# Optimization experiments

Hardware: AMD Instinct MI355X
Metric: run time of the kernel (lower is better)

Reference implementation:

```python
import jax, jax.numpy as jnp
import numpy as np
import math
from jax import lax

EPS = 1e-5  # BatchNorm1d default eps
K = 7       # causal conv kernel size
H = 5       # number of heads in block 2


def _cconv(x, w, b):
    # CausalConv1d: left-pad by (K-1)*dilation = 6, then valid conv. x: [B,C,L], w: [O,I,K]
    y = lax.conv_general_dilated(x, w, window_strides=(1,), padding=[(K - 1, 0)],
                                 dimension_numbers=('NCH', 'OIH', 'NCH'))
    return y + b[None, :, None]


def _bn(x, g, b):
    # BatchNorm1d in training mode: batch stats over (N, L) per channel, biased variance
    m = x.mean((0, 2), keepdims=True)
    v = ((x - m) ** 2).mean((0, 2), keepdims=True)
    return g[None, :, None] * (x - m) * lax.rsqrt(v + EPS) + b[None, :, None]


def _attn(x1, x2, x3, scale):
    # sigmoid(((X1 @ X2^T) / sqrt(L)) @ X3); x*: [B,C,L]
    s = jnp.einsum('bcl,bdl->bcd', x1, x2) * scale
    return jax.nn.sigmoid(jnp.einsum('bcd,bdl->bcl', s, x3))


def _attn_heads(x1, x2, x3, scale):
    # 5 heads chunked along L (contiguous chunks) -> vectorized over head axis
    B, C, L = x1.shape
    r = lambda x: x.reshape(B, C, H, L // H)
    x1r, x2r, x3r = r(x1), r(x2), r(x3)
    s = jnp.einsum('bchk,bdhk->bhcd', x1r, x2r) * scale  # scale uses full L, as in source
    a = jax.nn.sigmoid(jnp.einsum('bhcd,bdhk->bchk', s, x3r))
    return a.reshape(B, C, L)


def setup_inputs() -> dict:
    key = jax.random.key(0)
    ks = jax.random.split(key, 20)
    B, C, L = 64, 30, 200
    CL = C * L
    cs = (C * K) ** -0.5   # conv weight scale
    ls = CL ** -0.5        # linear weight scale
    d = {}
    d['X'] = jax.random.normal(ks[0], (B, C, L), jnp.float32)
    for i, nm in enumerate(['b1c1', 'b1c2', 'b1c3', 'b2c1', 'b2c2', 'b2c3']):
        d[nm + '_w'] = jax.random.normal(ks[1 + i], (C, C, K), jnp.float32) * cs
        d[nm + '_b'] = jax.random.normal(ks[7 + i], (C,), jnp.float32) * cs
    for nm in ['bn11', 'bn12', 'bn21', 'bn22']:
        d[nm + '_g'] = jnp.ones((C,), jnp.float32)
        d[nm + '_b'] = jnp.zeros((C,), jnp.float32)
    d['lin1_w'] = jax.random.normal(ks[13], (CL, CL), jnp.float32) * ls
    d['lin1_b'] = jax.random.normal(ks[14], (CL,), jnp.float32) * ls
    d['lin2_w'] = jax.random.normal(ks[15], (CL, CL), jnp.float32) * ls
    d['lin2_b'] = jax.random.normal(ks[16], (CL,), jnp.float32) * ls
    d['cw'] = jax.random.normal(ks[17], (CL, 2 * CL), jnp.float32) * (2 * CL) ** -0.5
    d['cb'] = jax.random.normal(ks[18], (CL,), jnp.float32) * (2 * CL) ** -0.5
    return d


def reference(X, b1c1_w, b1c1_b, b1c2_w, b1c2_b, b1c3_w, b1c3_b,
              bn11_g, bn11_b, lin1_w, lin1_b, lin2_w, lin2_b, bn12_g, bn12_b,
              b2c1_w, b2c1_b, b2c2_w, b2c2_b, b2c3_w, b2c3_b,
              bn21_g, bn21_b, bn22_g, bn22_b, cw, cb):
    B, C, L = X.shape
    scale = 1.0 / math.sqrt(L)
    # block 1: single-head sigmoid attention
    a1 = _attn(_cconv(X, b1c1_w, b1c1_b), _cconv(X, b1c2_w, b1c2_b),
               _cconv(X, b1c3_w, b1c3_b), scale)
    a1 = _bn(a1 + X, bn11_g, bn11_b)
    a1f = a1.reshape(B, -1)
    o1 = (a1f @ lin1_w.T + lin1_b) @ lin2_w.T + lin2_b  # dropout is eval-mode identity
    out1 = _bn(a1 + o1.reshape(B, C, L), bn12_g, bn12_b)
    # block 2: 5-head sigmoid attention
    a2 = _attn_heads(_cconv(X, b2c1_w, b2c1_b), _cconv(X, b2c2_w, b2c2_b),
                     _cconv(X, b2c3_w, b2c3_b), scale)
    a2 = _bn(a2 + X, bn21_g, bn21_b)
    a2f = a2.reshape(B, -1)
    # NOTE: source reuses b1_linearchain for block 2 (b2_linearchain is unused)
    o2 = (a2f @ lin1_w.T + lin1_b) @ lin2_w.T + lin2_b
    out2 = _bn(a2 + o2.reshape(B, C, L), bn22_g, bn22_b)
    # converge
    out = jnp.concatenate([out1, out2], axis=1).reshape(B, -1)  # [B, 2*C*L]
    out = out @ cw.T + cb                                       # [B, C*L]
    return out.reshape(B, 30, -1)
```

## Files before the change

### kernel.cpp

```cpp
#include <hip/hip_runtime.h>
#include <hip/hip_bf16.h>
#include <math.h>

typedef __attribute__((ext_vector_type(4))) float f32x4;
typedef __attribute__((ext_vector_type(8))) __bf16 bf16x8;
typedef __attribute__((ext_vector_type(8))) unsigned short u16x8;

__device__ __forceinline__ unsigned short f2bfu(float f) {
    unsigned u = __builtin_bit_cast(unsigned, f);
    u += 0x7fffu + ((u >> 16) & 1u);
    return (unsigned short)(u >> 16);
}

__device__ __forceinline__ bf16x8 to_bf8(f32x4 x, f32x4 y) {
    bf16x8 o;
#pragma unroll
    for (int j = 0; j < 4; ++j) { o[j] = (__bf16)x[j]; o[j + 4] = (__bf16)y[j]; }
    return o;
}

__device__ __forceinline__ void gload_lds16(const void* g, void* l) {
    __builtin_amdgcn_global_load_lds(
        (__attribute__((address_space(1))) const void*)g,
        (__attribute__((address_space(3))) void*)l, 16, 0, 0);
}

template <int VMPS>
__device__ __forceinline__ void wait_newer(int newer) {
    if (newer >= 2) {
        if constexpr (VMPS == 4) asm volatile("s_waitcnt vmcnt(8)" ::: "memory");
        else                     asm volatile("s_waitcnt vmcnt(6)" ::: "memory");
    } else if (newer == 1) {
        if constexpr (VMPS == 4) asm volatile("s_waitcnt vmcnt(4)" ::: "memory");
        else                     asm volatile("s_waitcnt vmcnt(3)" ::: "memory");
    } else {
        asm volatile("s_waitcnt vmcnt(0)" ::: "memory");
    }
}

struct ConvArgs {
    const float* w[6];
    const float* b[6];
};

__global__ __launch_bounds__(256) void conv_all(const float* __restrict__ X,
                                                ConvArgs args,
                                                float* __restrict__ out) {
    __shared__ float Xsp[30][208];
    __shared__ float Wg[30][212];
    const int b = blockIdx.x, j = blockIdx.y;
    const int tid = threadIdx.x;
    const float* xb = X + (size_t)b * 6000;
    for (int i = tid; i < 30 * 208; i += 256) {
        const int ci = i / 208, p = i - ci * 208;
        float v = 0.f;
        if (p >= 6 && p < 206) v = xb[ci * 200 + (p - 6)];
        Xsp[ci][p] = v;
    }
    const float* wsrc = args.w[j];
    for (int i = tid; i < 6300; i += 256) Wg[i / 210][i % 210] = wsrc[i];
    __syncthreads();
    if (tid < 240) {
        const int c = tid >> 3;
        const int strip = tid & 7;
        const int l0 = strip * 25;
        float acc[25];
        const float bias = args.b[j][c];
#pragma unroll
        for (int o = 0; o < 25; ++o) acc[o] = bias;
        for (int ci = 0; ci < 30; ++ci) {
            float wv[7];
#pragma unroll
            for (int kk = 0; kk < 7; ++kk) wv[kk] = Wg[c][ci * 7 + kk];
            float xw[31];
#pragma unroll
            for (int i = 0; i < 31; ++i) xw[i] = Xsp[ci][l0 + i];
#pragma unroll
            for (int o = 0; o < 25; ++o) {
                float a = acc[o];
#pragma unroll
                for (int kk = 0; kk < 7; ++kk) a += xw[o + kk] * wv[kk];
                acc[o] = a;
            }
        }
        float* op = out + ((size_t)j * 64 + b) * 6000 + c * 200 + l0;
#pragma unroll
        for (int o = 0; o < 25; ++o) op[o] = acc[o];
    }
}

__global__ __launch_bounds__(256) void attn_k(const float* __restrict__ conv,
                                              const float* __restrict__ X,
                                              float* __restrict__ A_lin) {
    __shared__ float x1s[30][204], x2s[30][204], x3s[30][204];
    __shared__ float S[5][30][30];
    const int b = blockIdx.x, blk = blockIdx.y;
    const int tid = threadIdx.x;
    const f32x4* c1 = (const f32x4*)(conv + (((size_t)blk * 3 + 0) * 64 + b) * 6000);
    const f32x4* c2 = (const f32x4*)(conv + (((size_t)blk * 3 + 1) * 64 + b) * 6000);
    const f32x4* c3 = (const f32x4*)(conv + (((size_t)blk * 3 + 2) * 64 + b) * 6000);
    for (int i = tid; i < 1500; i += 256) {
        const int c = i / 50, q = i - c * 50;
        *(f32x4*)&x1s[c][q * 4] = c1[i];
        *(f32x4*)&x2s[c][q * 4] = c2[i];
        *(f32x4*)&x3s[c][q * 4] = c3[i];
    }
    __syncthreads();
    const float scale = 7.0710678118654752e-2f;
    if (blk == 0) {
        for (int idx = tid; idx < 900; idx += 256) {
            const int c = idx / 30, d = idx - c * 30;
            f32x4 a4 = {};
            for (int q = 0; q < 50; ++q) {
                const f32x4 x = *(const f32x4*)&x1s[c][q * 4];
                const f32x4 y = *(const f32x4*)&x2s[d][q * 4];
                a4 += x * y;
            }
            S[0][c][d] = (a4[0] + a4[1] + a4[2] + a4[3]) * scale;
        }
    } else {
        for (int idx = tid; idx < 4500; idx += 256) {
            const int h = idx / 900, rem = idx - h * 900;
            const int c = rem / 30, d = rem - c * 30;
            f32x4 a4 = {};
            for (int q = 0; q < 10; ++q) {
                const f32x4 x = *(const f32x4*)&x1s[c][h * 40 + q * 4];
                const f32x4 y = *(const f32x4*)&x2s[d][h * 40 + q * 4];
                a4 += x * y;
            }
            S[h][c][d] = (a4[0] + a4[1] + a4[2] + a4[3]) * scale;
        }
    }
    __syncthreads();
    const float* Xb = X + (size_t)b * 6000;
    float* Ab = A_lin + ((size_t)blk * 64 + b) * 6000;
    for (int u = tid; u < 1500; u += 256) {
        const int c = u / 50, q = u - c * 50;
        const int hh = (blk == 0) ? 0 : (q / 10);
        f32x4 a4 = {};
        for (int d = 0; d < 30; ++d) {
            const float sv = S[hh][c][d];
            const f32x4 v = *(const f32x4*)&x3s[d][q * 4];
            a4 += sv * v;
        }
        const f32x4 xv = *(const f32x4*)(Xb + c * 200 + q * 4);
        f32x4 o;
#pragma unroll
        for (int jj = 0; jj < 4; ++jj)
            o[jj] = 1.f / (1.f + __expf(-a4[jj])) + xv[jj];
        *(f32x4*)(Ab + c * 200 + q * 4) = o;
    }
}

__global__ __launch_bounds__(256) void bn_stage1(float* __restrict__ A,
                                                 unsigned short* __restrict__ Ab,
                                                 const float* __restrict__ g11,
                                                 const float* __restrict__ b11,
                                                 const float* __restrict__ g21,
                                                 const float* __restrict__ b21) {
    const int c = blockIdx.x, h = blockIdx.y;
    const int tid = threadIdx.x;
    const size_t base = (size_t)h * 64 * 6000 + c * 200;
    float s = 0.f, ss = 0.f;
    for (int i = tid; i < 12800; i += 256) {
        const int b = i / 200, l = i - b * 200;
        const float v = A[base + (size_t)b * 6000 + l];
        s += v; ss += v * v;
    }
    __shared__ float rs[4], rss[4];
    __shared__ float sc_sh, sh_sh;
    for (int off = 32; off > 0; off >>= 1) { s += __shfl_down(s, off); ss += __shfl_down(ss, off); }
    const int wave = tid >> 6, lane = tid & 63;
    if (lane == 0) { rs[wave] = s; rss[wave] = ss; }
    __syncthreads();
    if (tid == 0) {
        const float S = rs[0] + rs[1] + rs[2] + rs[3];
        const float SS = rss[0] + rss[1] + rss[2] + rss[3];
        const float mean = S * (1.f / 12800.f);
        const float var = SS * (1.f / 12800.f) - mean * mean;
        const float* gp = h ? g21 : g11;
        const float* bp = h ? b21 : b11;
        const float scale = gp[c] * rsqrtf(var + 1e-5f);
        sc_sh = scale;
        sh_sh = bp[c] - mean * scale;
    }
    __syncthreads();
    const float scale = sc_sh, shift = sh_sh;
    for (int i = tid; i < 12800; i += 256) {
        const int b = i / 200, l = i - b * 200;
        const size_t idx = base + (size_t)b * 6000 + l;
        const float o = A[idx] * scale + shift;
        A[idx] = o;
        Ab[(size_t)(h * 64 + b) * 6016 + c * 200 + l] = f2bfu(o);
    }
    if (c == 0) {
        for (int i = tid; i < 64 * 16; i += 256)
            Ab[(size_t)(h * 64 + (i >> 4)) * 6016 + 6000 + (i & 15)] = 0;
    }
}

__global__ __launch_bounds__(256) void bn_stage2(const float* __restrict__ A,
                                                 const float* __restrict__ O,
                                                 unsigned short* __restrict__ Cat,
                                                 const float* __restrict__ g12,
                                                 const float* __restrict__ b12,
                                                 const float* __restrict__ g22,
                                                 const float* __restrict__ b22) {
    const int c = blockIdx.x, h = blockIdx.y;
    const int tid = threadIdx.x;
    const size_t base = (size_t)h * 64 * 6000 + c * 200;
    float s = 0.f, ss = 0.f;
    for (int i = tid; i < 12800; i += 256) {
        const int b = i / 200, l = i - b * 200;
        const size_t idx = base + (size_t)b * 6000 + l;
        const float v = A[idx] + O[idx];
        s += v; ss += v * v;
    }
    __shared__ float rs[4], rss[4];
    __shared__ float sc_sh, sh_sh;
    for (int off = 32; off > 0; off >>= 1) { s += __shfl_down(s, off); ss += __shfl_down(ss, off); }
    const int wave = tid >> 6, lane = tid & 63;
    if (lane == 0) { rs[wave] = s; rss[wave] = ss; }
    __syncthreads();
    if (tid == 0) {
        const float S = rs[0] + rs[1] + rs[2] + rs[3];
        const float SS = rss[0] + rss[1] + rss[2] + rss[3];
        const float mean = S * (1.f / 12800.f);
        const float var = SS * (1.f / 12800.f) - mean * mean;
        const float* gp = h ? g22 : g12;
        const float* bp = h ? b22 : b12;
        const float scale = gp[c] * rsqrtf(var + 1e-5f);
        sc_sh = scale;
        sh_sh = bp[c] - mean * scale;
    }
    __syncthreads();
    const float scale = sc_sh, shift = sh_sh;
    for (int i = tid; i < 12800; i += 256) {
        const int b = i / 200, l = i - b * 200;
        const size_t idx = base + (size_t)b * 6000 + l;
        const float o = (A[idx] + O[idx]) * scale + shift;
        Cat[(size_t)b * 12000 + (size_t)h * 6000 + c * 200 + l] = f2bfu(o);
    }
}

template <int MT>
__global__ __launch_bounds__(256) void gemm_pipe(const unsigned short* __restrict__ A,
                                                 const float* __restrict__ W,
                                                 unsigned short* __restrict__ P,
                                                 int N, int K, int KA,
                                                 int iters_total, int iters_per) {
    constexpr int M = MT * 16;
    constexpr int WB = 64 * 32 * 4;
    constexpr int AB = M * 32 * 2;
    constexpr int ACH = AB / 1024;
    constexpr int BUFSZ = WB + AB;
    constexpr int VMPS = 2 + ACH / 4;
    __shared__ __align__(16) char lds[3][BUFSZ];

    const int tid = threadIdx.x;
    const int wave = tid >> 6;
    const int lane = tid & 63;
    const int r = lane & 15;
    const int g = lane >> 4;
    const int n0 = blockIdx.x * 64;
    const int s = blockIdx.y;
    const int it0 = s * iters_per;
    int it1 = it0 + iters_per;
    if (it1 > iters_total) it1 = iters_total;
    const int nst = it1 - it0;

    f32x4 acc[MT] = {};

    auto stage = [&](char* base, int it) {
        const int k0 = it * 32;
#pragma unroll
        for (int u = 0; u < 2; ++u) {
            const int c = wave + 4 * u;
            const int slot = c * 64 + lane;
            const int row = slot >> 3, jj = slot & 7;
            const int j = jj ^ (row & 7);
            int kc = k0 + j * 4;
            if (kc + 4 > K) kc = K - 4;
            int rn = n0 + row;
            if (rn > N - 1) rn = N - 1;
            gload_lds16(W + (size_t)rn * K + kc, base + c * 1024);
        }
        char* abase = base + WB;
#pragma unroll
        for (int u = 0; u < ACH / 4; ++u) {
            const int c = wave + 4 * u;
            const int slot = c * 64 + lane;
            const int m = slot >> 2, jj = slot & 3;
            const int j = jj ^ ((m >> 1) & 3);
            const int kc = k0 + j * 8;
            gload_lds16(A + (size_t)m * KA + kc, abase + c * 1024);
        }
    };

    auto compute = [&](const char* base) {
        const float* Wb = (const float*)base;
        const unsigned short* Ab = (const unsigned short*)(base + WB);
        const int wr = wave * 16 + r;
        const f32x4* Wrow = (const f32x4*)(Wb + wr * 32);
        const f32x4 x = Wrow[(2 * g) ^ (r & 7)];
        const f32x4 y = Wrow[(2 * g + 1) ^ (r & 7)];
        const bf16x8 bfrag = to_bf8(x, y);
#pragma unroll
        for (int mt = 0; mt < MT; ++mt) {
            const int m = mt * 16 + r;
            const bf16x8 afrag = __builtin_bit_cast(
                bf16x8, ((const u16x8*)(Ab + (size_t)m * 32))[g ^ ((m >> 1) & 3)]);
            acc[mt] = __builtin_amdgcn_mfma_f32_16x16x32_bf16(afrag, bfrag, acc[mt], 0, 0, 0);
        }
    };

    if (nst > 0) {
        const int p = nst < 3 ? nst : 3;
        for (int i = 0; i < p; ++i) stage(&lds[i][0], it0 + i);
        wait_newer<VMPS>(p - 1);
        __builtin_amdgcn_s_barrier();
        __builtin_amdgcn_sched_barrier(0);

        int bi = 0;
        for (int it = it0; it < it1; ++it) {
            compute(&lds[bi][0]);
            __builtin_amdgcn_sched_barrier(0);
            __builtin_amdgcn_s_barrier();
            if (it + 3 < it1) stage(&lds[bi][0], it + 3);
            if (it + 1 < it1) {
                const int newer = (it + 3 <= it1 - 1) ? 2 : (it1 - 1) - (it + 1);
                wait_newer<VMPS>(newer);
                __builtin_amdgcn_s_barrier();
                __builtin_amdgcn_sched_barrier(0);
            }
            bi = bi == 2 ? 0 : bi + 1;
        }
    }

    unsigned short* Pp = P + (size_t)s * M * N;
    const int col = n0 + wave * 16 + r;
#pragma unroll
    for (int mt = 0; mt < MT; ++mt) {
#pragma unroll
        for (int rr = 0; rr < 4; ++rr) {
            const int row = mt * 16 + g * 4 + rr;
            if (col < N) Pp[(size_t)row * N + col] = f2bfu(acc[mt][rr]);
        }
    }
}

template <bool OUT_BF16>
__global__ __launch_bounds__(256) void reduce_bias(const unsigned short* __restrict__ P,
                                                   const float* __restrict__ bias,
                                                   int KS, int MN, int N, int KOUT,
                                                   float* __restrict__ of,
                                                   unsigned short* __restrict__ ob) {
    const int gid0 = blockIdx.x * 256 + threadIdx.x;
    const int gstr = gridDim.x * 256;
    for (int idx = gid0; idx < MN; idx += gstr) {
        float v = bias[idx % N];
        for (int s = 0; s < KS; ++s) {
            const unsigned u = P[(size_t)s * MN + idx];
            v += __builtin_bit_cast(float, u << 16);
        }
        if constexpr (OUT_BF16) ob[(size_t)(idx / N) * KOUT + (idx % N)] = f2bfu(v);
        else of[idx] = v;
    }
    if constexpr (OUT_BF16) {
        if (KOUT > N) {
            const int M = MN / N, PADW = KOUT - N;
            for (int i = gid0; i < M * PADW; i += gstr)
                ob[(size_t)(i / PADW) * KOUT + N + (i % PADW)] = 0;
        }
    }
}

extern "C" void kernel_launch(void* const* d_in, const int* in_sizes, int n_in,
                              void* d_out, int out_size, void* d_ws, size_t ws_size,
                              hipStream_t stream) {
    (void)in_sizes; (void)n_in; (void)out_size;
    const float* X = (const float*)d_in[0];
    ConvArgs ca;
    for (int j = 0; j < 6; ++j) {
        ca.w[j] = (const float*)d_in[1 + 2 * j];
        ca.b[j] = (const float*)d_in[2 + 2 * j];
    }
    const float* bn11_g = (const float*)d_in[13];
    const float* bn11_b = (const float*)d_in[14];
    const float* bn12_g = (const float*)d_in[15];
    const float* bn12_b = (const float*)d_in[16];
    const float* bn21_g = (const float*)d_in[17];
    const float* bn21_b = (const float*)d_in[18];
    const float* bn22_g = (const float*)d_in[19];
    const float* bn22_b = (const float*)d_in[20];
    const float* lin1_w = (const float*)d_in[21];
    const float* lin1_b = (const float*)d_in[22];
    const float* lin2_w = (const float*)d_in[23];
    const float* lin2_b = (const float*)d_in[24];
    const float* cw = (const float*)d_in[25];
    const float* cb = (const float*)d_in[26];
    float* out = (float*)d_out;

    char* w = (char*)d_ws;
    float* A_lin = (float*)w;
    unsigned short* A_bf = (unsigned short*)(w + 3072000);
    char* U = w + 4612096;
    float* convout = (float*)U;
    unsigned short* T_bf = (unsigned short*)U;
    float* O = (float*)(U + 1540096);
    unsigned short* Cat = (unsigned short*)(U + 4612096);
    unsigned short* P = (unsigned short*)(w + 13828096);

    const size_t avail = ws_size > 13828096 ? ws_size - 13828096 : 0;
    int KS12 = (int)(avail / 1536000);
    if (KS12 > 8) KS12 = 8;
    if (KS12 < 1) KS12 = 1;
    int KS3 = (int)(avail / 768000);
    if (KS3 > 10) KS3 = 10;
    if (KS3 < 1) KS3 = 1;

    conv_all<<<dim3(64, 6), 256, 0, stream>>>(X, ca, convout);
    attn_k<<<dim3(64, 2), 256, 0, stream>>>(convout, X, A_lin);
    bn_stage1<<<dim3(30, 2), 256, 0, stream>>>(A_lin, A_bf, bn11_g, bn11_b, bn21_g, bn21_b);

    {
        const int it_tot = 188;
        const int it_per = (it_tot + KS12 - 1) / KS12;
        gemm_pipe<8><<<dim3(94, KS12), 256, 0, stream>>>(A_bf, lin1_w, P, 6000, 6000, 6016, it_tot, it_per);
        reduce_bias<true><<<dim3(768), 256, 0, stream>>>(P, lin1_b, KS12, 768000, 6000, 6016, nullptr, T_bf);
        gemm_pipe<8><<<dim3(94, KS12), 256, 0, stream>>>(T_bf, lin2_w, P, 6000, 6000, 6016, it_tot, it_per);
        reduce_bias<false><<<dim3(768), 256, 0, stream>>>(P, lin2_b, KS12, 768000, 6000, 6000, O, nullptr);
    }

    bn_stage2<<<dim3(30, 2), 256, 0, stream>>>(A_lin, O, Cat, bn12_g, bn12_b, bn22_g, bn22_b);

    {
        const int it_tot = 375;
        const int it_per = (it_tot + KS3 - 1) / KS3;
        gemm_pipe<4><<<dim3(94, KS3), 256, 0, stream>>>(Cat, cw, P, 6000, 12000, 12000, it_tot, it_per);
        reduce_bias<false><<<dim3(768), 256, 0, stream>>>(P, cb, KS3, 384000, 6000, 6000, out, nullptr);
    }
}
```

Measured before the change: 282.5 us.

## Widen GEMM N-tile to 128, double-buffer, split BN into stats/apply

The GEMM now has each block cover 128 output columns instead of 64. Each wave holds two B fragments, so every A fragment read from LDS feeds two MFMAs. The pipeline goes from three LDS buffers to two, and the split-K caps rise to 12 and 16 to keep enough blocks with half as many N tiles. BatchNorm is split into a partial-statistics kernel and an apply kernel over a 30x2x8 grid instead of 60 blocks, so the bandwidth-bound normalization uses more CUs. In exchange the pipeline prefetches less deeply, the reduce kernels read more partial sums, and the GEMM uses more accumulator registers.

```diff
diff --git a/kernel.cpp b/kernel.cpp
--- a/kernel.cpp
+++ b/kernel.cpp
@@ -25,17 +25,11 @@
         (__attribute__((address_space(3))) void*)l, 16, 0, 0);
 }
 
-template <int VMPS>
-__device__ __forceinline__ void wait_newer(int newer) {
-    if (newer >= 2) {
-        if constexpr (VMPS == 4) asm volatile("s_waitcnt vmcnt(8)" ::: "memory");
-        else                     asm volatile("s_waitcnt vmcnt(6)" ::: "memory");
-    } else if (newer == 1) {
-        if constexpr (VMPS == 4) asm volatile("s_waitcnt vmcnt(4)" ::: "memory");
-        else                     asm volatile("s_waitcnt vmcnt(3)" ::: "memory");
-    } else {
-        asm volatile("s_waitcnt vmcnt(0)" ::: "memory");
-    }
+template <int N>
+__device__ __forceinline__ void waitcnt_vm() {
+    if constexpr (N == 6)      asm volatile("s_waitcnt vmcnt(6)" ::: "memory");
+    else if constexpr (N == 5) asm volatile("s_waitcnt vmcnt(5)" ::: "memory");
+    else                       asm volatile("s_waitcnt vmcnt(0)" ::: "memory");
 }
 
 struct ConvArgs {
@@ -152,92 +146,89 @@
     }
 }
 
-__global__ __launch_bounds__(256) void bn_stage1(float* __restrict__ A,
+template <bool ADD>
+__global__ __launch_bounds__(256) void bn_stats(const float* __restrict__ A,
+                                                const float* __restrict__ O,
+                                                float* __restrict__ part) {
+    const int c = blockIdx.x, h = blockIdx.y, bs = blockIdx.z;
+    const int tid = threadIdx.x;
+    float s = 0.f, ss = 0.f;
+    for (int i = tid; i < 1600; i += 256) {
+        const int b = bs * 8 + i / 200, l = i % 200;
+        const size_t idx = ((size_t)h * 64 + b) * 6000 + c * 200 + l;
+        float v = A[idx];
+        if constexpr (ADD) v += O[idx];
+        s += v; ss += v * v;
+    }
+    for (int off = 32; off > 0; off >>= 1) { s += __shfl_down(s, off); ss += __shfl_down(ss, off); }
+    __shared__ float rs[4], rss[4];
+    const int wave = tid >> 6, lane = tid & 63;
+    if (lane == 0) { rs[wave] = s; rss[wave] = ss; }
+    __syncthreads();
+    if (tid == 0) {
+        float* p = part + (((size_t)h * 30 + c) * 8 + bs) * 2;
+        p[0] = rs[0] + rs[1] + rs[2] + rs[3];
+        p[1] = rss[0] + rss[1] + rss[2] + rss[3];
+    }
+}
+
+__global__ __launch_bounds__(256) void bn_apply1(float* __restrict__ A,
                                                  unsigned short* __restrict__ Ab,
+                                                 const float* __restrict__ part,
                                                  const float* __restrict__ g11,
                                                  const float* __restrict__ b11,
                                                  const float* __restrict__ g21,
                                                  const float* __restrict__ b21) {
-    const int c = blockIdx.x, h = blockIdx.y;
-    const int tid = threadIdx.x;
-    const size_t base = (size_t)h * 64 * 6000 + c * 200;
-    float s = 0.f, ss = 0.f;
-    for (int i = tid; i < 12800; i += 256) {
-        const int b = i / 200, l = i - b * 200;
-        const float v = A[base + (size_t)b * 6000 + l];
-        s += v; ss += v * v;
-    }
-    __shared__ float rs[4], rss[4];
-    __shared__ float sc_sh, sh_sh;
-    for (int off = 32; off > 0; off >>= 1) { s += __shfl_down(s, off); ss += __shfl_down(ss, off); }
-    const int wave = tid >> 6, lane = tid & 63;
-    if (lane == 0) { rs[wave] = s; rss[wave] = ss; }
-    __syncthreads();
-    if (tid == 0) {
-        const float S = rs[0] + rs[1] + rs[2] + rs[3];
-        const float SS = rss[0] + rss[1] + rss[2] + rss[3];
-        const float mean = S * (1.f / 12800.f);
-        const float var = SS * (1.f / 12800.f) - mean * mean;
-        const float* gp = h ? g21 : g11;
-        const float* bp = h ? b21 : b11;
-        const float scale = gp[c] * rsqrtf(var + 1e-5f);
-        sc_sh = scale;
-        sh_sh = bp[c] - mean * scale;
-    }
-    __syncthreads();
-    const float scale = sc_sh, shift = sh_sh;
-    for (int i = tid; i < 12800; i += 256) {
-        const int b = i / 200, l = i - b * 200;
-        const size_t idx = base + (size_t)b * 6000 + l;
+    const int c = blockIdx.x, h = blockIdx.y, bs = blockIdx.z;
+    const int tid = threadIdx.x;
+    const float* p = part + (((size_t)h * 30 + c) * 8) * 2;
+    float S = 0.f, SS = 0.f;
+#pragma unroll
+    for (int k = 0; k < 8; ++k) { S += p[k * 2]; SS += p[k * 2 + 1]; }
+    const float mean = S * (1.f / 12800.f);
+    const float var = SS * (1.f / 12800.f) - mean * mean;
+    const float* gp = h ? g21 : g11;
+    const float* bp = h ? b21 : b11;
+    const float scale = gp[c] * rsqrtf(var + 1e-5f);
+    const float shift = bp[c] - mean * scale;
+    for (int i = tid; i < 1600; i += 256) {
+        const int b = bs * 8 + i / 200, l = i % 200;
+        const size_t idx = ((size_t)h * 64 + b) * 6000 + c * 200 + l;
         const float o = A[idx] * scale + shift;
         A[idx] = o;
-        Ab[(size_t)(h * 64 + b) * 6016 + c * 200 + l] = f2bfu(o);
+        Ab[((size_t)h * 64 + b) * 6016 + c * 200 + l] = f2bfu(o);
     }
     if (c == 0) {
-        for (int i = tid; i < 64 * 16; i += 256)
-            Ab[(size_t)(h * 64 + (i >> 4)) * 6016 + 6000 + (i & 15)] = 0;
-    }
-}
-
-__global__ __launch_bounds__(256) void bn_stage2(const float* __restrict__ A,
+        for (int i = tid; i < 8 * 16; i += 256) {
+            const int b = bs * 8 + (i >> 4);
+            Ab[((size_t)h * 64 + b) * 6016 + 6000 + (i & 15)] = 0;
+        }
+    }
+}
+
+__global__ __launch_bounds__(256) void bn_apply2(const float* __restrict__ A,
                                                  const float* __restrict__ O,
                                                  unsigned short* __restrict__ Cat,
+                                                 const float* __restrict__ part,
                                                  const float* __restrict__ g12,
                                                  const float* __restrict__ b12,
                                                  const float* __restrict__ g22,
                                                  const float* __restrict__ b22) {
-    const int c = blockIdx.x, h = blockIdx.y;
-    const int tid = threadIdx.x;
-    const size_t base = (size_t)h * 64 * 6000 + c * 200;
-    float s = 0.f, ss = 0.f;
-    for (int i = tid; i < 12800; i += 256) {
-        const int b = i / 200, l = i - b * 200;
-        const size_t idx = base + (size_t)b * 6000 + l;
-        const float v = A[idx] + O[idx];
-        s += v; ss += v * v;
-    }
-    __shared__ float rs[4], rss[4];
-    __shared__ float sc_sh, sh_sh;
-    for (int off = 32; off > 0; off >>= 1) { s += __shfl_down(s, off); ss += __shfl_down(ss, off); }
-    const int wave = tid >> 6, lane = tid & 63;
-    if (lane == 0) { rs[wave] = s; rss[wave] = ss; }
-    __syncthreads();
-    if (tid == 0) {
-        const float S = rs[0] + rs[1] + rs[2] + rs[3];
-        const float SS = rss[0] + rss[1] + rss[2] + rss[3];
-        const float mean = S * (1.f / 12800.f);
-        const float var = SS * (1.f / 12800.f) - mean * mean;
-        const float* gp = h ? g22 : g12;
-        const float* bp = h ? b22 : b12;
-        const float scale = gp[c] * rsqrtf(var + 1e-5f);
-        sc_sh = scale;
-        sh_sh = bp[c] - mean * scale;
-    }
-    __syncthreads();
-    const float scale = sc_sh, shift = sh_sh;
-    for (int i = tid; i < 12800; i += 256) {
-        const int b = i / 200, l = i - b * 200;
-        const size_t idx = base + (size_t)b * 6000 + l;
+    const int c = blockIdx.x, h = blockIdx.y, bs = blockIdx.z;
+    const int tid = threadIdx.x;
+    const float* p = part + (((size_t)h * 30 + c) * 8) * 2;
+    float S = 0.f, SS = 0.f;
+#pragma unroll
+    for (int k = 0; k < 8; ++k) { S += p[k * 2]; SS += p[k * 2 + 1]; }
+    const float mean = S * (1.f / 12800.f);
+    const float var = SS * (1.f / 12800.f) - mean * mean;
+    const float* gp = h ? g22 : g12;
+    const float* bp = h ? b22 : b12;
+    const float scale = gp[c] * rsqrtf(var + 1e-5f);
+    const float shift = bp[c] - mean * scale;
+    for (int i = tid; i < 1600; i += 256) {
+        const int b = bs * 8 + i / 200, l = i % 200;
+        const size_t idx = ((size_t)h * 64 + b) * 6000 + c * 200 + l;
         const float o = (A[idx] + O[idx]) * scale + shift;
         Cat[(size_t)b * 12000 + (size_t)h * 6000 + c * 200 + l] = f2bfu(o);
     }
@@ -250,31 +241,31 @@
                                                  int N, int K, int KA,
                                                  int iters_total, int iters_per) {
     constexpr int M = MT * 16;
-    constexpr int WB = 64 * 32 * 4;
+    constexpr int WB = 128 * 32 * 4;
     constexpr int AB = M * 32 * 2;
     constexpr int ACH = AB / 1024;
     constexpr int BUFSZ = WB + AB;
-    constexpr int VMPS = 2 + ACH / 4;
-    __shared__ __align__(16) char lds[3][BUFSZ];
+    constexpr int VMPS = 4 + ACH / 4;
+    __shared__ __align__(16) char lds[2][BUFSZ];
 
     const int tid = threadIdx.x;
     const int wave = tid >> 6;
     const int lane = tid & 63;
     const int r = lane & 15;
     const int g = lane >> 4;
-    const int n0 = blockIdx.x * 64;
+    const int n0 = blockIdx.x * 128;
     const int s = blockIdx.y;
     const int it0 = s * iters_per;
     int it1 = it0 + iters_per;
     if (it1 > iters_total) it1 = iters_total;
     const int nst = it1 - it0;
 
-    f32x4 acc[MT] = {};
+    f32x4 acc[MT][2] = {};
 
     auto stage = [&](char* base, int it) {
         const int k0 = it * 32;
 #pragma unroll
-        for (int u = 0; u < 2; ++u) {
+        for (int u = 0; u < 4; ++u) {
             const int c = wave + 4 * u;
             const int slot = c * 64 + lane;
             const int row = slot >> 3, jj = slot & 7;
@@ -300,51 +291,63 @@
     auto compute = [&](const char* base) {
         const float* Wb = (const float*)base;
         const unsigned short* Ab = (const unsigned short*)(base + WB);
-        const int wr = wave * 16 + r;
-        const f32x4* Wrow = (const f32x4*)(Wb + wr * 32);
-        const f32x4 x = Wrow[(2 * g) ^ (r & 7)];
-        const f32x4 y = Wrow[(2 * g + 1) ^ (r & 7)];
-        const bf16x8 bfrag = to_bf8(x, y);
+        bf16x8 bfrag[2];
+#pragma unroll
+        for (int nt = 0; nt < 2; ++nt) {
+            const int wr = (wave + 4 * nt) * 16 + r;
+            const f32x4* Wrow = (const f32x4*)(Wb + wr * 32);
+            bfrag[nt] = to_bf8(Wrow[(2 * g) ^ (r & 7)], Wrow[(2 * g + 1) ^ (r & 7)]);
+        }
 #pragma unroll
         for (int mt = 0; mt < MT; ++mt) {
             const int m = mt * 16 + r;
             const bf16x8 afrag = __builtin_bit_cast(
                 bf16x8, ((const u16x8*)(Ab + (size_t)m * 32))[g ^ ((m >> 1) & 3)]);
-            acc[mt] = __builtin_amdgcn_mfma_f32_16x16x32_bf16(afrag, bfrag, acc[mt], 0, 0, 0);
+            acc[mt][0] = __builtin_amdgcn_mfma_f32_16x16x32_bf16(afrag, bfrag[0], acc[mt][0], 0, 0, 0);
+            acc[mt][1] = __builtin_amdgcn_mfma_f32_16x16x32_bf16(afrag, bfrag[1], acc[mt][1], 0, 0, 0);
         }
     };
 
     if (nst > 0) {
-        const int p = nst < 3 ? nst : 3;
-        for (int i = 0; i < p; ++i) stage(&lds[i][0], it0 + i);
-        wait_newer<VMPS>(p - 1);
+        stage(&lds[0][0], it0);
+        if (nst > 1) {
+            stage(&lds[1][0], it0 + 1);
+            waitcnt_vm<VMPS>();
+        } else {
+            waitcnt_vm<0>();
+        }
         __builtin_amdgcn_s_barrier();
         __builtin_amdgcn_sched_barrier(0);
 
-        int bi = 0;
+        int cur = 0;
         for (int it = it0; it < it1; ++it) {
-            compute(&lds[bi][0]);
+            compute(&lds[cur][0]);
             __builtin_amdgcn_sched_barrier(0);
             __builtin_amdgcn_s_barrier();
-            if (it + 3 < it1) stage(&lds[bi][0], it + 3);
+            if (it + 2 < it1) stage(&lds[cur][0], it + 2);
             if (it + 1 < it1) {
-                const int newer = (it + 3 <= it1 - 1) ? 2 : (it1 - 1) - (it + 1);
-                wait_newer<VMPS>(newer);
+                if (it + 2 < it1) waitcnt_vm<VMPS>();
+                else              waitcnt_vm<0>();
                 __builtin_amdgcn_s_barrier();
                 __builtin_amdgcn_sched_barrier(0);
             }
-            bi = bi == 2 ? 0 : bi + 1;
+            cur ^= 1;
         }
     }
 
     unsigned short* Pp = P + (size_t)s * M * N;
-    const int col = n0 + wave * 16 + r;
-#pragma unroll
-    for (int mt = 0; mt < MT; ++mt) {
-#pragma unroll
-        for (int rr = 0; rr < 4; ++rr) {
-            const int row = mt * 16 + g * 4 + rr;
-            if (col < N) Pp[(size_t)row * N + col] = f2bfu(acc[mt][rr]);
+#pragma unroll
+    for (int nt = 0; nt < 2; ++nt) {
+        const int col = n0 + (wave + 4 * nt) * 16 + r;
+        if (col < N) {
+#pragma unroll
+            for (int mt = 0; mt < MT; ++mt) {
+#pragma unroll
+                for (int rr = 0; rr < 4; ++rr) {
+                    const int row = mt * 16 + g * 4 + rr;
+                    Pp[(size_t)row * N + col] = f2bfu(acc[mt][nt][rr]);
+                }
+            }
         }
     }
 }
@@ -409,35 +412,38 @@
     unsigned short* T_bf = (unsigned short*)U;
     float* O = (float*)(U + 1540096);
     unsigned short* Cat = (unsigned short*)(U + 4612096);
-    unsigned short* P = (unsigned short*)(w + 13828096);
-
-    const size_t avail = ws_size > 13828096 ? ws_size - 13828096 : 0;
+    float* BNS = (float*)(w + 13828096);
+    unsigned short* P = (unsigned short*)(w + 13832192);
+
+    const size_t avail = ws_size > 13832192 ? ws_size - 13832192 : 0;
     int KS12 = (int)(avail / 1536000);
-    if (KS12 > 8) KS12 = 8;
+    if (KS12 > 12) KS12 = 12;
     if (KS12 < 1) KS12 = 1;
     int KS3 = (int)(avail / 768000);
-    if (KS3 > 10) KS3 = 10;
+    if (KS3 > 16) KS3 = 16;
     if (KS3 < 1) KS3 = 1;
 
     conv_all<<<dim3(64, 6), 256, 0, stream>>>(X, ca, convout);
     attn_k<<<dim3(64, 2), 256, 0, stream>>>(convout, X, A_lin);
-    bn_stage1<<<dim3(30, 2), 256, 0, stream>>>(A_lin, A_bf, bn11_g, bn11_b, bn21_g, bn21_b);
+    bn_stats<false><<<dim3(30, 2, 8), 256, 0, stream>>>(A_lin, nullptr, BNS);
+    bn_apply1<<<dim3(30, 2, 8), 256, 0, stream>>>(A_lin, A_bf, BNS, bn11_g, bn11_b, bn21_g, bn21_b);
 
     {
         const int it_tot = 188;
         const int it_per = (it_tot + KS12 - 1) / KS12;
-        gemm_pipe<8><<<dim3(94, KS12), 256, 0, stream>>>(A_bf, lin1_w, P, 6000, 6000, 6016, it_tot, it_per);
+        gemm_pipe<8><<<dim3(47, KS12), 256, 0, stream>>>(A_bf, lin1_w, P, 6000, 6000, 6016, it_tot, it_per);
         reduce_bias<true><<<dim3(768), 256, 0, stream>>>(P, lin1_b, KS12, 768000, 6000, 6016, nullptr, T_bf);
-        gemm_pipe<8><<<dim3(94, KS12), 256, 0, stream>>>(T_bf, lin2_w, P, 6000, 6000, 6016, it_tot, it_per);
+        gemm_pipe<8><<<dim3(47, KS12), 256, 0, stream>>>(T_bf, lin2_w, P, 6000, 6000, 6016, it_tot, it_per);
         reduce_bias<false><<<dim3(768), 256, 0, stream>>>(P, lin2_b, KS12, 768000, 6000, 6000, O, nullptr);
     }
 
-    bn_stage2<<<dim3(30, 2), 256, 0, stream>>>(A_lin, O, Cat, bn12_g, bn12_b, bn22_g, bn22_b);
+    bn_stats<true><<<dim3(30, 2, 8), 256, 0, stream>>>(A_lin, O, BNS);
+    bn_apply2<<<dim3(30, 2, 8), 256, 0, stream>>>(A_lin, O, Cat, BNS, bn12_g, bn12_b, bn22_g, bn22_b);
 
     {
         const int it_tot = 375;
         const int it_per = (it_tot + KS3 - 1) / KS3;
-        gemm_pipe<4><<<dim3(94, KS3), 256, 0, stream>>>(Cat, cw, P, 6000, 12000, 12000, it_tot, it_per);
+        gemm_pipe<4><<<dim3(47, KS3), 256, 0, stream>>>(Cat, cw, P, 6000, 12000, 12000, it_tot, it_per);
         reduce_bias<false><<<dim3(768), 256, 0, stream>>>(P, cb, KS3, 384000, 6000, 6000, out, nullptr);
     }
 }
```

After: 261.8 us. -7.3%, faster.
